# Performance work log

Measured on AMD Instinct MI355X. Metric: run time of the kernel, lower is better.

The kernel has to match this reference:

```python
import jax, jax.numpy as jnp
import numpy as np

N = 100000
E = 1600000
F_IN = 128
H = 128


def gcn_conv(x, src, dst, w, b):
    # PyG GCNConv: add self-loops, symmetric deg^{-1/2} normalization,
    # out = scatter_add(norm[e] * (x @ W)[src[e]], dst[e]) + bias
    n = x.shape[0]
    h = x @ w  # [N, H]
    deg = jax.ops.segment_sum(jnp.ones_like(dst, dtype=h.dtype), dst, num_segments=n) + 1.0  # +1 self-loop
    dinv = jax.lax.rsqrt(deg)  # [N]
    norm = dinv[src] * dinv[dst]  # [E]
    agg = jax.ops.segment_sum(h[src] * norm[:, None], dst, num_segments=n)
    agg = agg + h * (dinv * dinv)[:, None]  # self-loop term
    return agg + b


def setup_inputs() -> dict:
    key = jax.random.key(0)
    ks = jax.random.split(key, 9)
    x = jax.random.normal(ks[0], (N, F_IN), dtype=jnp.float32)
    edge_index = jax.random.randint(ks[1], (2, E), 0, N, dtype=jnp.int64)
    concentration = jax.random.uniform(ks[2], (N,), dtype=jnp.float32)
    s = 1.0 / np.sqrt(F_IN)
    w1 = jax.random.normal(ks[3], (F_IN, H), dtype=jnp.float32) * s
    b1 = jax.random.normal(ks[4], (H,), dtype=jnp.float32) * 0.01
    w2 = jax.random.normal(ks[5], (H, H), dtype=jnp.float32) * (1.0 / np.sqrt(H))
    b2 = jax.random.normal(ks[6], (H,), dtype=jnp.float32) * 0.01
    fc_w = jax.random.normal(ks[7], (2 * H, 1), dtype=jnp.float32) * (1.0 / np.sqrt(2 * H))
    fc_b = jax.random.normal(ks[8], (1,), dtype=jnp.float32) * 0.01
    return {"x": x, "edge_index": edge_index, "concentration": concentration,
            "w1": w1, "b1": b1, "w2": w2, "b2": b2, "fc_w": fc_w, "fc_b": fc_b}


def reference(x, edge_index, concentration, w1, b1, w2, b2, fc_w, fc_b):
    src, dst = edge_index[0], edge_index[1]
    h = jax.nn.relu(gcn_conv(x, src, dst, w1, b1))
    h = jax.nn.relu(gcn_conv(h, src, dst, w2, b2))
    target_idx = 0
    target_features = h[target_idx]  # [H]
    mask = (dst == target_idx).astype(h.dtype)  # [E]
    cnt = jnp.maximum(mask.sum(), 1.0)
    # mean of h[src] over edges pointing at the target node
    neighbor_features = jnp.einsum('e,eh->h', mask, h[src]) / cnt  # [H]
    combined = jnp.concatenate([target_features, neighbor_features])  # [2H]
    out = combined @ fc_w + fc_b  # [1]
    return out.reshape(-1)
```

## Files before the change

### kernel.cpp

```cpp
#include <hip/hip_runtime.h>
#include <math.h>

#define N_NODES 100000

#define C_NS   0
#define C_NT   1
#define C_DONE 2

#define S_CAP   128
#define T_CAP   1024
#define BCAP    64
#define NBW     ((N_NODES + 31) / 32)

#define G1_BLOCKS 48
#define NS_MAX    G1_BLOCKS


__global__ __launch_bounds__(256) void passA_kernel(const int* __restrict__ src,
                                                    const int* __restrict__ dst,
                                                    int* ctr,
                                                    unsigned* __restrict__ Sbits,
                                                    unsigned* __restrict__ Tbits,
                                                    unsigned* __restrict__ Mbits,
                                                    int* Slist, int* Tlist, int* bcnt,
                                                    const float* __restrict__ fcb,
                                                    float* __restrict__ out, int e) {
    int gtid = blockIdx.x * 256 + threadIdx.x;
    int gstr = gridDim.x * 256;
    if (gtid == 0) {
        Slist[0] = 0; Tlist[0] = 0; bcnt[0] = 0;
        out[0] = fcb[0];
    }
    for (int i = gtid; i < NBW; i += gstr) { Tbits[i] = 0u; Mbits[i] = 0u; }
    auto body = [&](int d, int i) {
        if (d == 0) {
            int s = src[i];
            if (s != 0) {
                unsigned bit = 1u << (s & 31);
                unsigned old = atomicOr(&Sbits[s >> 5], bit);
                if (!(old & bit)) {
                    int k = 1 + atomicAdd(&ctr[C_NS], 1);
                    if (k < S_CAP) Slist[k] = s;
                }
            }
        }
    };
    bool al = ((((unsigned long long)(const void*)dst) & 15ull) == 0ull);
    int nv4 = al ? (e >> 2) : 0;
    for (int q = gtid; q < nv4; q += gstr) {
        int4 dv = ((const int4*)dst)[q];
        int b = q << 2;
        body(dv.x, b); body(dv.y, b + 1); body(dv.z, b + 2); body(dv.w, b + 3);
    }
    for (int i = (nv4 << 2) + gtid; i < e; i += gstr) body(dst[i], i);
}

__global__ __launch_bounds__(256) void passB_kernel(const int* __restrict__ src,
                                                    const int* __restrict__ dst,
                                                    const unsigned* __restrict__ Sbits,
                                                    unsigned* __restrict__ Tbits,
                                                    int* __restrict__ mapT,
                                                    int* Tlist, int* bcnt, int* ctr, int e) {
    int gtid = blockIdx.x * 256 + threadIdx.x;
    int gstr = gridDim.x * 256;
    auto body = [&](int d, int i) {
        bool inS = (d == 0) || ((Sbits[d >> 5] >> (d & 31)) & 1u);
        if (inS) {
            int s = src[i];
            if (s != 0) {
                unsigned bit = 1u << (s & 31);
                unsigned old = atomicOr(&Tbits[s >> 5], bit);
                if (!(old & bit)) {
                    int k = 1 + atomicAdd(&ctr[C_NT], 1);
                    if (k < T_CAP) { Tlist[k] = s; bcnt[k] = 0; mapT[s] = k; }
                    else mapT[s] = T_CAP;
                }
            }
        }
    };
    bool al = ((((unsigned long long)(const void*)dst) & 15ull) == 0ull);
    int nv4 = al ? (e >> 2) : 0;
    for (int q = gtid; q < nv4; q += gstr) {
        int4 dv = ((const int4*)dst)[q];
        int b = q << 2;
        body(dv.x, b); body(dv.y, b + 1); body(dv.z, b + 2); body(dv.w, b + 3);
    }
    for (int i = (nv4 << 2) + gtid; i < e; i += gstr) body(dst[i], i);
}

__global__ __launch_bounds__(256) void passC_kernel(const int* __restrict__ src,
                                                    const int* __restrict__ dst,
                                                    const unsigned* __restrict__ Tbits,
                                                    const int* __restrict__ mapT,
                                                    unsigned* __restrict__ Mbits,
                                                    int* __restrict__ cnt,
                                                    int* __restrict__ bcnt,
                                                    int* __restrict__ bucket, int e) {
    int gtid = blockIdx.x * 256 + threadIdx.x;
    int gstr = gridDim.x * 256;
    auto body = [&](int d, int i) {
        bool inT = (d == 0) || ((Tbits[d >> 5] >> (d & 31)) & 1u);
        if (inT) {
            int r = (d == 0) ? 0 : mapT[d];
            if (r < T_CAP) {
                int s = src[i];
                int slot = atomicAdd(&bcnt[r], 1);
                if (slot < BCAP) bucket[r * BCAP + slot] = s;
                unsigned bit = 1u << (s & 31);
                unsigned old = atomicOr(&Mbits[s >> 5], bit);
                if (!(old & bit)) cnt[s] = 0;
            }
        }
    };
    bool al = ((((unsigned long long)(const void*)dst) & 15ull) == 0ull);
    int nv4 = al ? (e >> 2) : 0;
    for (int q = gtid; q < nv4; q += gstr) {
        int4 dv = ((const int4*)dst)[q];
        int b = q << 2;
        body(dv.x, b); body(dv.y, b + 1); body(dv.z, b + 2); body(dv.w, b + 3);
    }
    for (int i = (nv4 << 2) + gtid; i < e; i += gstr) body(dst[i], i);
}

__global__ __launch_bounds__(256) void passD_kernel(const int* __restrict__ dst,
                                                    const unsigned* __restrict__ Mbits,
                                                    int* __restrict__ cnt, int e) {
    int gtid = blockIdx.x * 256 + threadIdx.x;
    int gstr = gridDim.x * 256;
    auto body = [&](int d) {
        if ((Mbits[d >> 5] >> (d & 31)) & 1u) atomicAdd(&cnt[d], 1);
    };
    bool al = ((((unsigned long long)(const void*)dst) & 15ull) == 0ull);
    int nv4 = al ? (e >> 2) : 0;
    for (int q = gtid; q < nv4; q += gstr) {
        int4 dv = ((const int4*)dst)[q];
        body(dv.x); body(dv.y); body(dv.z); body(dv.w);
    }
    for (int i = (nv4 << 2) + gtid; i < e; i += gstr) body(dst[i]);
}

__global__ __launch_bounds__(512) void fused_kernel(const float* __restrict__ x,
                                                    const int* __restrict__ Tlist,
                                                    const int* __restrict__ Slist,
                                                    const int* __restrict__ bcnt,
                                                    const int* __restrict__ bucket,
                                                    const int* __restrict__ cnt,
                                                    const int* __restrict__ mapT,
                                                    int* ctr,
                                                    const float* __restrict__ W1,
                                                    const float* __restrict__ b1,
                                                    const float* __restrict__ W2,
                                                    const float* __restrict__ b2,
                                                    const float* __restrict__ fcw,
                                                    float* __restrict__ h1out,
                                                    float* __restrict__ out) {
    __shared__ float sW[128 * 128];
    __shared__ float sRow[8][128];
    __shared__ int   sTr2[BCAP];
    __shared__ float sWt2[BCAP];
    __shared__ float sPart[4][128];
    __shared__ float sAgg2[128];
    __shared__ float sMult2;
    __shared__ float sRed[2];

    int tid = threadIdx.x;
    int nT = ctr[C_NT] + 1; if (nT > T_CAP) nT = T_CAP;

    for (int i = tid; i < 128 * 32; i += 512)
        ((float4*)sW)[i] = ((const float4*)W1)[i];
    __syncthreads();

    int wave = tid >> 6, lane = tid & 63;
    for (int r0 = blockIdx.x * 8; r0 < nT; r0 += G1_BLOCKS * 8) {
        int r = r0 + wave;
        if (r < nT) {
            int v = Tlist[r];
            int degd = bcnt[r];
            int nb = degd < BCAP ? degd : BCAP;
            float dinv_d = rsqrtf((float)degd + 1.0f);
            int   sj = (lane < nb) ? bucket[r * BCAP + lane] : 0;
            float wj = (lane < nb) ? dinv_d * rsqrtf((float)cnt[sj] + 1.0f) : 0.f;
            float selfw = 1.0f / ((float)degd + 1.0f);
            float2 a0 = ((const float2*)(x + (long)v * 128))[lane];
            float2 accA = { selfw * a0.x, selfw * a0.y };
            float2 accB = { 0.f, 0.f };
            int j = 0;
            for (; j + 2 <= nb; j += 2) {
                int   s0 = __shfl(sj, j),     s1 = __shfl(sj, j + 1);
                float w0 = __shfl(wj, j),     w1 = __shfl(wj, j + 1);
                float2 a = ((const float2*)(x + (long)s0 * 128))[lane];
                float2 b = ((const float2*)(x + (long)s1 * 128))[lane];
                accA.x += w0 * a.x; accA.y += w0 * a.y;
                accB.x += w1 * b.x; accB.y += w1 * b.y;
            }
            if (j < nb) {
                int   s0 = __shfl(sj, j);
                float w0 = __shfl(wj, j);
                float2 a = ((const float2*)(x + (long)s0 * 128))[lane];
                accA.x += w0 * a.x; accA.y += w0 * a.y;
            }
            sRow[wave][2 * lane]     = accA.x + accB.x;
            sRow[wave][2 * lane + 1] = accA.y + accB.y;
        }
        __syncthreads();
        if (r < nT) {
            float o0 = 0.f, o1 = 0.f;
#pragma unroll 8
            for (int k = 0; k < 128; ++k) {
                float rv = sRow[wave][k];
                o0 = fmaf(rv, sW[k * 128 + lane], o0);
                o1 = fmaf(rv, sW[k * 128 + 64 + lane], o1);
            }
            h1out[(long)r * 128 + lane]      = fmaxf(o0 + b1[lane], 0.f);
            h1out[(long)r * 128 + 64 + lane] = fmaxf(o1 + b1[64 + lane], 0.f);
        }
        __syncthreads();
    }

    int nS = ctr[C_NS] + 1; if (nS > NS_MAX) nS = NS_MAX;
    __threadfence();
    __syncthreads();
    if (tid == 0)
        __hip_atomic_fetch_add(&ctr[C_DONE], 1, __ATOMIC_RELEASE, __HIP_MEMORY_SCOPE_AGENT);
    if ((int)blockIdx.x >= nS) return;
    if (tid == 0) {
        while (__hip_atomic_load(&ctr[C_DONE], __ATOMIC_ACQUIRE,
                                 __HIP_MEMORY_SCOPE_AGENT) < G1_BLOCKS)
            __builtin_amdgcn_s_sleep(2);
    }
    __syncthreads();
    __threadfence();

    int rb = blockIdx.x;
    int part = tid >> 7;
    int c = tid & 127;

    int v = Slist[rb];
    int trv = (v == 0) ? 0 : mapT[v];
    if (trv < 0 || trv >= T_CAP) trv = 0;
    int degv = bcnt[trv];
    int nb = degv < BCAP ? degv : BCAP;
    float dinv_v = rsqrtf((float)degv + 1.0f);
    if (tid < nb) {
        int s = bucket[trv * BCAP + tid];
        int ts = (s == 0) ? 0 : mapT[s];
        if (ts < 0 || ts >= T_CAP) ts = 0;
        sTr2[tid] = ts;
        sWt2[tid] = dinv_v * rsqrtf((float)bcnt[ts] + 1.0f);
    }
    int ne0t = bcnt[0];
    int ne0c = ne0t < BCAP ? ne0t : BCAP;
    {
        bool eq = (tid < ne0c) && (bucket[tid] == v);
        unsigned long long m = __ballot(eq);
        if (tid == 0) sMult2 = (float)__popcll(m);
    }
    __syncthreads();

    float a = (part == 0) ? (1.0f / ((float)degv + 1.0f)) * h1out[(long)trv * 128 + c] : 0.f;
    for (int j = part; j < nb; j += 4)
        a = fmaf(sWt2[j], h1out[(long)sTr2[j] * 128 + c], a);
    sPart[part][c] = a;
    __syncthreads();
    if (part == 0)
        sAgg2[c] = sPart[0][c] + sPart[1][c] + sPart[2][c] + sPart[3][c];
    __syncthreads();

    float g = 0.f;
    int k0 = part * 32;
#pragma unroll 8
    for (int k = k0; k < k0 + 32; ++k)
        g = fmaf(sAgg2[k], W2[k * 128 + c], g);
    sPart[part][c] = g;
    __syncthreads();

    if (part == 0) {
        float h2c = fmaxf(sPart[0][c] + sPart[1][c] + sPart[2][c] + sPart[3][c] + b2[c], 0.f);
        float mdiv = (float)(ne0t < 1 ? 1 : ne0t);
        float val = (sMult2 / mdiv) * h2c * fcw[128 + c];
        if (rb == 0) val += h2c * fcw[c];
        for (int o = 32; o > 0; o >>= 1) val += __shfl_down(val, o);
        if ((tid & 63) == 0) sRed[tid >> 6] = val;
    }
    __syncthreads();
    if (tid == 0) atomicAdd(out, sRed[0] + sRed[1]);
}

extern "C" void kernel_launch(void* const* d_in, const int* in_sizes, int n_in,
                              void* d_out, int out_size, void* d_ws, size_t ws_size,
                              hipStream_t stream) {
    const float* x   = (const float*)d_in[0];
    const int*   ei  = (const int*)d_in[1];
    const float* w1  = (const float*)d_in[3];
    const float* b1  = (const float*)d_in[4];
    const float* w2  = (const float*)d_in[5];
    const float* b2  = (const float*)d_in[6];
    const float* fcw = (const float*)d_in[7];
    const float* fcb = (const float*)d_in[8];

    const int n = N_NODES;
    const int e = in_sizes[1] / 2;
    const int* src = ei;
    const int* dst = ei + e;

    char* ws = (char*)d_ws;
    size_t off = 0;
    auto take = [&](size_t bytes) -> void* {
        void* p = ws + off;
        off += (bytes + 255) & ~(size_t)255;
        return p;
    };
    int*      ctr   = (int*)take(64 * 4);
    unsigned* Sbits = (unsigned*)take((size_t)NBW * 4);
    size_t zero_bytes = off;
    unsigned* Tbits = (unsigned*)take((size_t)NBW * 4);
    unsigned* Mbits = (unsigned*)take((size_t)NBW * 4);
    int*      cnt   = (int*)take((size_t)n * 4);
    int*      bcnt  = (int*)take((size_t)T_CAP * 4);
    int*   Slist  = (int*)take((size_t)S_CAP * 4);
    int*   Tlist  = (int*)take((size_t)T_CAP * 4);
    int*   mapT   = (int*)take((size_t)n * 4);
    int*   bucket = (int*)take((size_t)T_CAP * BCAP * 4);
    float* h1out  = (float*)take((size_t)T_CAP * 128 * 4);
    (void)ws_size;

    hipMemsetAsync(ws, 0, zero_bytes, stream);

    passA_kernel<<<1024, 256, 0, stream>>>(src, dst, ctr, Sbits, Tbits, Mbits,
                                           Slist, Tlist, bcnt, fcb, (float*)d_out, e);
    passB_kernel<<<1024, 256, 0, stream>>>(src, dst, Sbits, Tbits, mapT, Tlist,
                                           bcnt, ctr, e);
    passC_kernel<<<1024, 256, 0, stream>>>(src, dst, Tbits, mapT, Mbits, cnt,
                                           bcnt, bucket, e);
    passD_kernel<<<1024, 256, 0, stream>>>(dst, Mbits, cnt, e);

    fused_kernel<<<G1_BLOCKS, 512, 0, stream>>>(x, Tlist, Slist, bcnt, bucket, cnt,
                                                mapT, ctr, w1, b1, w2, b2, fcw,
                                                h1out, (float*)d_out);
}
```

Before: 150.9 us.

## Merge edge-scan passes and fused stage into one persistent kernel with grid barriers

Replaces four separate edge-scanning kernel launches plus the fused GCN kernel with a single persistent kernel of 256 blocks of 512 threads. Stages are separated by software grid barriers built on atomic counters in the workspace. This removes launch gaps and inter-kernel drain, but relies on all 256 blocks being co-resident. The edge passes now run on fewer threads (256x512 instead of 1024x256), and every block loads W1 into 64KB of shared memory, which may limit occupancy.

```diff
diff --git a/kernel.cpp b/kernel.cpp
--- a/kernel.cpp
+++ b/kernel.cpp
@@ -5,153 +5,51 @@
 
 #define C_NS   0
 #define C_NT   1
-#define C_DONE 2
+#define C_BAR  8
 
 #define S_CAP   128
 #define T_CAP   1024
 #define BCAP    64
 #define NBW     ((N_NODES + 31) / 32)
 
-#define G1_BLOCKS 48
-#define NS_MAX    G1_BLOCKS
-
-
-__global__ __launch_bounds__(256) void passA_kernel(const int* __restrict__ src,
+#define NBLK 256
+#define NTHR 512
+#define NS_MAX 48
+
+#define GBAR(slot)                                                                   \
+    do {                                                                             \
+        __threadfence();                                                             \
+        __syncthreads();                                                             \
+        if (tid == 0) {                                                              \
+            __hip_atomic_fetch_add(&ctr[slot], 1, __ATOMIC_ACQ_REL,                  \
+                                   __HIP_MEMORY_SCOPE_AGENT);                        \
+            while (__hip_atomic_load(&ctr[slot], __ATOMIC_ACQUIRE,                   \
+                                     __HIP_MEMORY_SCOPE_AGENT) < NBLK)               \
+                __builtin_amdgcn_s_sleep(1);                                         \
+        }                                                                            \
+        __syncthreads();                                                             \
+    } while (0)
+
+
+__global__ __launch_bounds__(NTHR) void mega_kernel(const float* __restrict__ x,
+                                                    const int* __restrict__ src,
                                                     const int* __restrict__ dst,
-                                                    int* ctr,
-                                                    unsigned* __restrict__ Sbits,
-                                                    unsigned* __restrict__ Tbits,
-                                                    unsigned* __restrict__ Mbits,
-                                                    int* Slist, int* Tlist, int* bcnt,
-                                                    const float* __restrict__ fcb,
-                                                    float* __restrict__ out, int e) {
-    int gtid = blockIdx.x * 256 + threadIdx.x;
-    int gstr = gridDim.x * 256;
-    if (gtid == 0) {
-        Slist[0] = 0; Tlist[0] = 0; bcnt[0] = 0;
-        out[0] = fcb[0];
-    }
-    for (int i = gtid; i < NBW; i += gstr) { Tbits[i] = 0u; Mbits[i] = 0u; }
-    auto body = [&](int d, int i) {
-        if (d == 0) {
-            int s = src[i];
-            if (s != 0) {
-                unsigned bit = 1u << (s & 31);
-                unsigned old = atomicOr(&Sbits[s >> 5], bit);
-                if (!(old & bit)) {
-                    int k = 1 + atomicAdd(&ctr[C_NS], 1);
-                    if (k < S_CAP) Slist[k] = s;
-                }
-            }
-        }
-    };
-    bool al = ((((unsigned long long)(const void*)dst) & 15ull) == 0ull);
-    int nv4 = al ? (e >> 2) : 0;
-    for (int q = gtid; q < nv4; q += gstr) {
-        int4 dv = ((const int4*)dst)[q];
-        int b = q << 2;
-        body(dv.x, b); body(dv.y, b + 1); body(dv.z, b + 2); body(dv.w, b + 3);
-    }
-    for (int i = (nv4 << 2) + gtid; i < e; i += gstr) body(dst[i], i);
-}
-
-__global__ __launch_bounds__(256) void passB_kernel(const int* __restrict__ src,
-                                                    const int* __restrict__ dst,
-                                                    const unsigned* __restrict__ Sbits,
-                                                    unsigned* __restrict__ Tbits,
-                                                    int* __restrict__ mapT,
-                                                    int* Tlist, int* bcnt, int* ctr, int e) {
-    int gtid = blockIdx.x * 256 + threadIdx.x;
-    int gstr = gridDim.x * 256;
-    auto body = [&](int d, int i) {
-        bool inS = (d == 0) || ((Sbits[d >> 5] >> (d & 31)) & 1u);
-        if (inS) {
-            int s = src[i];
-            if (s != 0) {
-                unsigned bit = 1u << (s & 31);
-                unsigned old = atomicOr(&Tbits[s >> 5], bit);
-                if (!(old & bit)) {
-                    int k = 1 + atomicAdd(&ctr[C_NT], 1);
-                    if (k < T_CAP) { Tlist[k] = s; bcnt[k] = 0; mapT[s] = k; }
-                    else mapT[s] = T_CAP;
-                }
-            }
-        }
-    };
-    bool al = ((((unsigned long long)(const void*)dst) & 15ull) == 0ull);
-    int nv4 = al ? (e >> 2) : 0;
-    for (int q = gtid; q < nv4; q += gstr) {
-        int4 dv = ((const int4*)dst)[q];
-        int b = q << 2;
-        body(dv.x, b); body(dv.y, b + 1); body(dv.z, b + 2); body(dv.w, b + 3);
-    }
-    for (int i = (nv4 << 2) + gtid; i < e; i += gstr) body(dst[i], i);
-}
-
-__global__ __launch_bounds__(256) void passC_kernel(const int* __restrict__ src,
-                                                    const int* __restrict__ dst,
-                                                    const unsigned* __restrict__ Tbits,
-                                                    const int* __restrict__ mapT,
-                                                    unsigned* __restrict__ Mbits,
-                                                    int* __restrict__ cnt,
-                                                    int* __restrict__ bcnt,
-                                                    int* __restrict__ bucket, int e) {
-    int gtid = blockIdx.x * 256 + threadIdx.x;
-    int gstr = gridDim.x * 256;
-    auto body = [&](int d, int i) {
-        bool inT = (d == 0) || ((Tbits[d >> 5] >> (d & 31)) & 1u);
-        if (inT) {
-            int r = (d == 0) ? 0 : mapT[d];
-            if (r < T_CAP) {
-                int s = src[i];
-                int slot = atomicAdd(&bcnt[r], 1);
-                if (slot < BCAP) bucket[r * BCAP + slot] = s;
-                unsigned bit = 1u << (s & 31);
-                unsigned old = atomicOr(&Mbits[s >> 5], bit);
-                if (!(old & bit)) cnt[s] = 0;
-            }
-        }
-    };
-    bool al = ((((unsigned long long)(const void*)dst) & 15ull) == 0ull);
-    int nv4 = al ? (e >> 2) : 0;
-    for (int q = gtid; q < nv4; q += gstr) {
-        int4 dv = ((const int4*)dst)[q];
-        int b = q << 2;
-        body(dv.x, b); body(dv.y, b + 1); body(dv.z, b + 2); body(dv.w, b + 3);
-    }
-    for (int i = (nv4 << 2) + gtid; i < e; i += gstr) body(dst[i], i);
-}
-
-__global__ __launch_bounds__(256) void passD_kernel(const int* __restrict__ dst,
-                                                    const unsigned* __restrict__ Mbits,
-                                                    int* __restrict__ cnt, int e) {
-    int gtid = blockIdx.x * 256 + threadIdx.x;
-    int gstr = gridDim.x * 256;
-    auto body = [&](int d) {
-        if ((Mbits[d >> 5] >> (d & 31)) & 1u) atomicAdd(&cnt[d], 1);
-    };
-    bool al = ((((unsigned long long)(const void*)dst) & 15ull) == 0ull);
-    int nv4 = al ? (e >> 2) : 0;
-    for (int q = gtid; q < nv4; q += gstr) {
-        int4 dv = ((const int4*)dst)[q];
-        body(dv.x); body(dv.y); body(dv.z); body(dv.w);
-    }
-    for (int i = (nv4 << 2) + gtid; i < e; i += gstr) body(dst[i]);
-}
-
-__global__ __launch_bounds__(512) void fused_kernel(const float* __restrict__ x,
-                                                    const int* __restrict__ Tlist,
-                                                    const int* __restrict__ Slist,
-                                                    const int* __restrict__ bcnt,
-                                                    const int* __restrict__ bucket,
-                                                    const int* __restrict__ cnt,
-                                                    const int* __restrict__ mapT,
-                                                    int* ctr,
+                                                    int e,
                                                     const float* __restrict__ W1,
                                                     const float* __restrict__ b1,
                                                     const float* __restrict__ W2,
                                                     const float* __restrict__ b2,
                                                     const float* __restrict__ fcw,
+                                                    const float* __restrict__ fcb,
+                                                    int* ctr,
+                                                    unsigned* __restrict__ Sbits,
+                                                    unsigned* __restrict__ Tbits,
+                                                    unsigned* __restrict__ Mbits,
+                                                    int* __restrict__ cnt,
+                                                    int* __restrict__ bcnt,
+                                                    int* Slist, int* Tlist,
+                                                    int* __restrict__ mapT,
+                                                    int* __restrict__ bucket,
                                                     float* __restrict__ h1out,
                                                     float* __restrict__ out) {
     __shared__ float sW[128 * 128];
@@ -163,75 +61,157 @@
     __shared__ float sMult2;
     __shared__ float sRed[2];
 
-    int tid = threadIdx.x;
-    int nT = ctr[C_NT] + 1; if (nT > T_CAP) nT = T_CAP;
-
-    for (int i = tid; i < 128 * 32; i += 512)
+    const int tid = threadIdx.x, bid = blockIdx.x;
+    const int gtid = bid * NTHR + tid;
+    const int gstr = NBLK * NTHR;
+
+    for (int i = tid; i < 128 * 32; i += NTHR)
         ((float4*)sW)[i] = ((const float4*)W1)[i];
-    __syncthreads();
-
-    int wave = tid >> 6, lane = tid & 63;
-    for (int r0 = blockIdx.x * 8; r0 < nT; r0 += G1_BLOCKS * 8) {
-        int r = r0 + wave;
-        if (r < nT) {
-            int v = Tlist[r];
-            int degd = bcnt[r];
-            int nb = degd < BCAP ? degd : BCAP;
-            float dinv_d = rsqrtf((float)degd + 1.0f);
-            int   sj = (lane < nb) ? bucket[r * BCAP + lane] : 0;
-            float wj = (lane < nb) ? dinv_d * rsqrtf((float)cnt[sj] + 1.0f) : 0.f;
-            float selfw = 1.0f / ((float)degd + 1.0f);
-            float2 a0 = ((const float2*)(x + (long)v * 128))[lane];
-            float2 accA = { selfw * a0.x, selfw * a0.y };
-            float2 accB = { 0.f, 0.f };
-            int j = 0;
-            for (; j + 2 <= nb; j += 2) {
-                int   s0 = __shfl(sj, j),     s1 = __shfl(sj, j + 1);
-                float w0 = __shfl(wj, j),     w1 = __shfl(wj, j + 1);
-                float2 a = ((const float2*)(x + (long)s0 * 128))[lane];
-                float2 b = ((const float2*)(x + (long)s1 * 128))[lane];
-                accA.x += w0 * a.x; accA.y += w0 * a.y;
-                accB.x += w1 * b.x; accB.y += w1 * b.y;
-            }
-            if (j < nb) {
-                int   s0 = __shfl(sj, j);
-                float w0 = __shfl(wj, j);
-                float2 a = ((const float2*)(x + (long)s0 * 128))[lane];
-                accA.x += w0 * a.x; accA.y += w0 * a.y;
-            }
-            sRow[wave][2 * lane]     = accA.x + accB.x;
-            sRow[wave][2 * lane + 1] = accA.y + accB.y;
-        }
-        __syncthreads();
-        if (r < nT) {
-            float o0 = 0.f, o1 = 0.f;
+
+    if (gtid == 0) { Slist[0] = 0; Tlist[0] = 0; bcnt[0] = 0; out[0] = fcb[0]; }
+    for (int i = gtid; i < NBW; i += gstr) { Tbits[i] = 0u; Mbits[i] = 0u; }
+
+    const bool al = ((((unsigned long long)(const void*)dst) & 15ull) == 0ull);
+    const int nv4 = al ? (e >> 2) : 0;
+
+    {
+        auto body = [&](int d, int i) {
+            if (d == 0) {
+                int s = src[i];
+                if (s != 0) {
+                    unsigned bit = 1u << (s & 31);
+                    unsigned old = atomicOr(&Sbits[s >> 5], bit);
+                    if (!(old & bit)) {
+                        int k = 1 + atomicAdd(&ctr[C_NS], 1);
+                        if (k < S_CAP) Slist[k] = s;
+                    }
+                }
+            }
+        };
+        for (int q = gtid; q < nv4; q += gstr) {
+            int4 dv = ((const int4*)dst)[q];
+            int b = q << 2;
+            body(dv.x, b); body(dv.y, b + 1); body(dv.z, b + 2); body(dv.w, b + 3);
+        }
+        for (int i = (nv4 << 2) + gtid; i < e; i += gstr) body(dst[i], i);
+    }
+    GBAR(C_BAR + 0);
+
+    {
+        auto body = [&](int d, int i) {
+            bool inS = (d == 0) || ((Sbits[d >> 5] >> (d & 31)) & 1u);
+            if (inS) {
+                int s = src[i];
+                if (s != 0) {
+                    unsigned bit = 1u << (s & 31);
+                    unsigned old = atomicOr(&Tbits[s >> 5], bit);
+                    if (!(old & bit)) {
+                        int k = 1 + atomicAdd(&ctr[C_NT], 1);
+                        if (k < T_CAP) { Tlist[k] = s; bcnt[k] = 0; mapT[s] = k; }
+                        else mapT[s] = T_CAP;
+                    }
+                }
+            }
+        };
+        for (int q = gtid; q < nv4; q += gstr) {
+            int4 dv = ((const int4*)dst)[q];
+            int b = q << 2;
+            body(dv.x, b); body(dv.y, b + 1); body(dv.z, b + 2); body(dv.w, b + 3);
+        }
+        for (int i = (nv4 << 2) + gtid; i < e; i += gstr) body(dst[i], i);
+    }
+    GBAR(C_BAR + 1);
+
+    {
+        auto body = [&](int d, int i) {
+            bool inT = (d == 0) || ((Tbits[d >> 5] >> (d & 31)) & 1u);
+            if (inT) {
+                int r = (d == 0) ? 0 : mapT[d];
+                if (r < T_CAP) {
+                    int s = src[i];
+                    int slot = atomicAdd(&bcnt[r], 1);
+                    if (slot < BCAP) bucket[r * BCAP + slot] = s;
+                    unsigned bit = 1u << (s & 31);
+                    unsigned old = atomicOr(&Mbits[s >> 5], bit);
+                    if (!(old & bit)) cnt[s] = 0;
+                }
+            }
+        };
+        for (int q = gtid; q < nv4; q += gstr) {
+            int4 dv = ((const int4*)dst)[q];
+            int b = q << 2;
+            body(dv.x, b); body(dv.y, b + 1); body(dv.z, b + 2); body(dv.w, b + 3);
+        }
+        for (int i = (nv4 << 2) + gtid; i < e; i += gstr) body(dst[i], i);
+    }
+    GBAR(C_BAR + 2);
+
+    {
+        auto body = [&](int d) {
+            if ((Mbits[d >> 5] >> (d & 31)) & 1u) atomicAdd(&cnt[d], 1);
+        };
+        for (int q = gtid; q < nv4; q += gstr) {
+            int4 dv = ((const int4*)dst)[q];
+            body(dv.x); body(dv.y); body(dv.z); body(dv.w);
+        }
+        for (int i = (nv4 << 2) + gtid; i < e; i += gstr) body(dst[i]);
+    }
+    GBAR(C_BAR + 3);
+
+    {
+        int nT = ctr[C_NT] + 1; if (nT > T_CAP) nT = T_CAP;
+        int wave = tid >> 6, lane = tid & 63;
+        for (int r0 = bid * 8; r0 < nT; r0 += NBLK * 8) {
+            int r = r0 + wave;
+            if (r < nT) {
+                int v = Tlist[r];
+                int degd = bcnt[r];
+                int nb = degd < BCAP ? degd : BCAP;
+                float dinv_d = rsqrtf((float)degd + 1.0f);
+                int   sj = (lane < nb) ? bucket[r * BCAP + lane] : 0;
+                float wj = (lane < nb) ? dinv_d * rsqrtf((float)cnt[sj] + 1.0f) : 0.f;
+                float selfw = 1.0f / ((float)degd + 1.0f);
+                float2 a0 = ((const float2*)(x + (long)v * 128))[lane];
+                float2 accA = { selfw * a0.x, selfw * a0.y };
+                float2 accB = { 0.f, 0.f };
+                int j = 0;
+                for (; j + 2 <= nb; j += 2) {
+                    int   s0 = __shfl(sj, j),     s1 = __shfl(sj, j + 1);
+                    float w0 = __shfl(wj, j),     w1 = __shfl(wj, j + 1);
+                    float2 a = ((const float2*)(x + (long)s0 * 128))[lane];
+                    float2 b = ((const float2*)(x + (long)s1 * 128))[lane];
+                    accA.x += w0 * a.x; accA.y += w0 * a.y;
+                    accB.x += w1 * b.x; accB.y += w1 * b.y;
+                }
+                if (j < nb) {
+                    int   s0 = __shfl(sj, j);
+                    float w0 = __shfl(wj, j);
+                    float2 a = ((const float2*)(x + (long)s0 * 128))[lane];
+                    accA.x += w0 * a.x; accA.y += w0 * a.y;
+                }
+                sRow[wave][2 * lane]     = accA.x + accB.x;
+                sRow[wave][2 * lane + 1] = accA.y + accB.y;
+            }
+            __syncthreads();
+            if (r < nT) {
+                float o0 = 0.f, o1 = 0.f;
 #pragma unroll 8
-            for (int k = 0; k < 128; ++k) {
-                float rv = sRow[wave][k];
-                o0 = fmaf(rv, sW[k * 128 + lane], o0);
-                o1 = fmaf(rv, sW[k * 128 + 64 + lane], o1);
-            }
-            h1out[(long)r * 128 + lane]      = fmaxf(o0 + b1[lane], 0.f);
-            h1out[(long)r * 128 + 64 + lane] = fmaxf(o1 + b1[64 + lane], 0.f);
-        }
-        __syncthreads();
-    }
+                for (int k = 0; k < 128; ++k) {
+                    float rv = sRow[wave][k];
+                    o0 = fmaf(rv, sW[k * 128 + lane], o0);
+                    o1 = fmaf(rv, sW[k * 128 + 64 + lane], o1);
+                }
+                h1out[(long)r * 128 + lane]      = fmaxf(o0 + b1[lane], 0.f);
+                h1out[(long)r * 128 + 64 + lane] = fmaxf(o1 + b1[64 + lane], 0.f);
+            }
+            __syncthreads();
+        }
+    }
+    GBAR(C_BAR + 4);
 
     int nS = ctr[C_NS] + 1; if (nS > NS_MAX) nS = NS_MAX;
-    __threadfence();
-    __syncthreads();
-    if (tid == 0)
-        __hip_atomic_fetch_add(&ctr[C_DONE], 1, __ATOMIC_RELEASE, __HIP_MEMORY_SCOPE_AGENT);
-    if ((int)blockIdx.x >= nS) return;
-    if (tid == 0) {
-        while (__hip_atomic_load(&ctr[C_DONE], __ATOMIC_ACQUIRE,
-                                 __HIP_MEMORY_SCOPE_AGENT) < G1_BLOCKS)
-            __builtin_amdgcn_s_sleep(2);
-    }
-    __syncthreads();
-    __threadfence();
-
-    int rb = blockIdx.x;
+    if (bid >= nS) return;
+    int rb = bid;
     int part = tid >> 7;
     int c = tid & 127;
 
@@ -326,15 +306,8 @@
 
     hipMemsetAsync(ws, 0, zero_bytes, stream);
 
-    passA_kernel<<<1024, 256, 0, stream>>>(src, dst, ctr, Sbits, Tbits, Mbits,
-                                           Slist, Tlist, bcnt, fcb, (float*)d_out, e);
-    passB_kernel<<<1024, 256, 0, stream>>>(src, dst, Sbits, Tbits, mapT, Tlist,
-                                           bcnt, ctr, e);
-    passC_kernel<<<1024, 256, 0, stream>>>(src, dst, Tbits, mapT, Mbits, cnt,
-                                           bcnt, bucket, e);
-    passD_kernel<<<1024, 256, 0, stream>>>(dst, Mbits, cnt, e);
-
-    fused_kernel<<<G1_BLOCKS, 512, 0, stream>>>(x, Tlist, Slist, bcnt, bucket, cnt,
-                                                mapT, ctr, w1, b1, w2, b2, fcw,
-                                                h1out, (float*)d_out);
+    mega_kernel<<<NBLK, NTHR, 0, stream>>>(x, src, dst, e, w1, b1, w2, b2, fcw, fcb,
+                                           ctr, Sbits, Tbits, Mbits, cnt, bcnt,
+                                           Slist, Tlist, mapT, bucket,
+                                           h1out, (float*)d_out);
 }
```

Result: slower. 405.8 us (+169.0%).
